# Performance work log

Hardware: AMD Instinct MI355X
Metric: run time of the kernel (lower is better)

The kernel has to match this reference:

```python
import jax, jax.numpy as jnp
import numpy as np

B, C, H, W = 4, 256, 64, 64
INTER = C // 2
BN_EPS = 1e-5


def setup_inputs() -> dict:
    key = jax.random.key(0)
    ks = jax.random.split(key, 12)
    s = 0.05
    return {
        "x": jax.random.normal(ks[0], (B, C, H, W), dtype=jnp.float32),
        "theta_w": jax.random.normal(ks[1], (INTER, C), dtype=jnp.float32) * s,
        "theta_b": jax.random.normal(ks[2], (INTER,), dtype=jnp.float32) * s,
        "phi_w": jax.random.normal(ks[3], (INTER, C), dtype=jnp.float32) * s,
        "phi_b": jax.random.normal(ks[4], (INTER,), dtype=jnp.float32) * s,
        "g_w": jax.random.normal(ks[5], (INTER, C), dtype=jnp.float32) * s,
        "g_b": jax.random.normal(ks[6], (INTER,), dtype=jnp.float32) * s,
        "W_w": jax.random.normal(ks[7], (C, INTER), dtype=jnp.float32) * s,
        "W_b": jax.random.normal(ks[8], (C,), dtype=jnp.float32) * s,
        "bn_gamma": jnp.ones((C,), dtype=jnp.float32),
        "bn_beta": jnp.zeros((C,), dtype=jnp.float32),
    }


def _conv1x1(x, w, b):
    # 1x1 conv == per-pixel GEMM: (B,C,H,W) x (O,C) -> (B,O,H,W)
    return jnp.einsum("bchw,oc->bohw", x, w) + b[None, :, None, None]


def reference(x, theta_w, theta_b, phi_w, phi_b, g_w, g_b, W_w, W_b, bn_gamma, bn_beta):
    b, c, h, w = x.shape
    hw = h * w
    theta = _conv1x1(x, theta_w, theta_b).reshape(b, -1, hw)  # (B, inter, HW) -> queries
    phi = _conv1x1(x, phi_w, phi_b).reshape(b, -1, hw)        # (B, inter, HW) -> keys
    g = _conv1x1(x, g_w, g_b).reshape(b, -1, hw)              # (B, inter, HW) -> values
    # f[n,m] = <theta[:,n], phi[:,m]> over all HW spatial positions
    f = jnp.einsum("bin,bim->bnm", theta, phi)                # (B, HW, HW)
    attn = jax.nn.softmax(f, axis=-1)
    y = jnp.einsum("bnm,bim->bin", attn, g)                   # (B, inter, HW)
    y = y.reshape(b, c // 2, h, w)
    wy = _conv1x1(y, W_w, W_b)                                # (B, C, H, W)
    # BatchNorm2d (training-mode batch statistics, per channel)
    mean = jnp.mean(wy, axis=(0, 2, 3), keepdims=True)
    var = jnp.var(wy, axis=(0, 2, 3), keepdims=True)
    wy_bn = bn_gamma[None, :, None, None] * (wy - mean) * jax.lax.rsqrt(var + BN_EPS) + bn_beta[None, :, None, None]
    return wy_bn + x
```

## Files before the change

kernel.cpp:

```cpp
#include <hip/hip_runtime.h>
#include <hip/hip_bf16.h>

#define HWN   4096
#define CIN   256
#define NINTER 128
#define NBATCH 4
#define BN_EPS 1e-5f
#define LOG2E 1.4426950408889634f
#define SMAX  64.0f

typedef __bf16 bf16_t;
typedef __bf16 bf16x8 __attribute__((ext_vector_type(8)));
typedef __bf16 bf16x4 __attribute__((ext_vector_type(4)));
typedef float  f32x4  __attribute__((ext_vector_type(4)));
typedef float  f32x16 __attribute__((ext_vector_type(16)));

__device__ __forceinline__ float fexp2(float x) {
  return __builtin_amdgcn_exp2f(x);
}

__device__ __forceinline__ void split_bf16(float v, bf16_t& h, bf16_t& l) {
  h = (bf16_t)v;
  l = (bf16_t)(v - (float)h);
}

__global__ __launch_bounds__(256) void convert_weights(
    const float* __restrict__ tw, const float* __restrict__ pw,
    const float* __restrict__ gw, const float* __restrict__ ww,
    bf16_t* __restrict__ out) {
  int i = blockIdx.x * 256 + threadIdx.x;
  float v;
  if (i < 32768)        v = tw[i];
  else if (i < 65536)   v = pw[i - 32768];
  else if (i < 98304)   v = gw[i - 65536];
  else                  v = ww[i - 98304];
  bf16_t h, l;
  split_bf16(v, h, l);
  out[i] = h;
  out[131072 + i] = l;
}

__global__ __launch_bounds__(256, 4) void qkv_kernel(
    const float* __restrict__ x, const bf16_t* __restrict__ wbf,
    const float* __restrict__ tb, const float* __restrict__ pb,
    const float* __restrict__ gb,
    bf16_t* __restrict__ Qh, bf16_t* __restrict__ Kh, bf16_t* __restrict__ V) {
  const int ntb  = blockIdx.x;
  const int b    = blockIdx.y;
  const int tid  = threadIdx.x;
  const int lane = tid & 63;
  const int wv   = tid >> 6;
  const int l31  = lane & 31;
  const int half = lane >> 5;

  __shared__ __align__(16) bf16_t smem[4608];
  bf16_t (*xTh)[72] = (bf16_t(*)[72])smem;
  bf16_t (*xTl)[72] = (bf16_t(*)[72])(smem + 2304);
  bf16_t (*Tr)[136] = (bf16_t(*)[136])smem;

  const bf16_t* Th = wbf;
  const bf16_t* Tl = wbf + 131072;
  const bf16_t* Ph = wbf + 32768;
  const bf16_t* Pl = wbf + 131072 + 32768;
  const bf16_t* Gh = wbf + 65536;
  const float*  xb = x + (size_t)b * CIN * HWN + ntb * 32;

  f32x16 aq, ak, av;
#pragma unroll
  for (int i = 0; i < 16; i++) { aq[i] = 0.f; ak[i] = 0.f; av[i] = 0.f; }

  for (int c0 = 0; c0 < 256; c0 += 64) {
    __syncthreads();
#pragma unroll
    for (int i = 0; i < 8; i++) {
      int idx = tid + i * 256;
      int cc = idx >> 5;
      int nn = idx & 31;
      float v = xb[(size_t)(c0 + cc) * HWN + nn];
      bf16_t h, l;
      split_bf16(v, h, l);
      xTh[nn][cc] = h;
      xTl[nn][cc] = l;
    }
    __syncthreads();
#pragma unroll
    for (int kk = 0; kk < 64; kk += 16) {
      size_t woff = (size_t)(32 * wv + l31) * 256 + c0 + kk + half * 8;
      bf16x8 th = *(const bf16x8*)(Th + woff);
      bf16x8 tl = *(const bf16x8*)(Tl + woff);
      bf16x8 ph = *(const bf16x8*)(Ph + woff);
      bf16x8 pl = *(const bf16x8*)(Pl + woff);
      bf16x8 gh = *(const bf16x8*)(Gh + woff);
      bf16x8 bh = *(const bf16x8*)(&xTh[l31][kk + half * 8]);
      bf16x8 bl = *(const bf16x8*)(&xTl[l31][kk + half * 8]);
      aq = __builtin_amdgcn_mfma_f32_32x32x16_bf16(th, bh, aq, 0, 0, 0);
      aq = __builtin_amdgcn_mfma_f32_32x32x16_bf16(th, bl, aq, 0, 0, 0);
      aq = __builtin_amdgcn_mfma_f32_32x32x16_bf16(tl, bh, aq, 0, 0, 0);
      ak = __builtin_amdgcn_mfma_f32_32x32x16_bf16(ph, bh, ak, 0, 0, 0);
      ak = __builtin_amdgcn_mfma_f32_32x32x16_bf16(ph, bl, ak, 0, 0, 0);
      ak = __builtin_amdgcn_mfma_f32_32x32x16_bf16(pl, bh, ak, 0, 0, 0);
      av = __builtin_amdgcn_mfma_f32_32x32x16_bf16(gh, bh, av, 0, 0, 0);
    }
  }

  const int trow = tid >> 3;
  const int tc16 = (tid & 7) * 16;
  bf16_t* qh = Qh + ((size_t)b * HWN + ntb * 32) * NINTER;
  bf16_t* kh = Kh + ((size_t)b * HWN + ntb * 32) * NINTER;

#pragma unroll
  for (int rnd = 0; rnd < 2; rnd++) {
    __syncthreads();
#pragma unroll
    for (int rg = 0; rg < 4; rg++) {
      int och0 = 32 * wv + 8 * rg + 4 * half;
#pragma unroll
      for (int j = 0; j < 4; j++) {
        float v = (rnd == 0) ? (aq[rg * 4 + j] + tb[och0 + j]) * LOG2E
                             : (ak[rg * 4 + j] + pb[och0 + j]);
        Tr[l31][och0 + j] = (bf16_t)v;
      }
    }
    __syncthreads();
    bf16_t* dst = (rnd == 0) ? qh : kh;
    bf16x8 v0 = *(const bf16x8*)(&Tr[trow][tc16]);
    bf16x8 v1 = *(const bf16x8*)(&Tr[trow][tc16 + 8]);
    *(bf16x8*)(dst + (size_t)trow * NINTER + tc16) = v0;
    *(bf16x8*)(dst + (size_t)trow * NINTER + tc16 + 8) = v1;
  }

  const int n = ntb * 32 + l31;
  bf16_t* vd = V + (size_t)b * NINTER * HWN;
#pragma unroll
  for (int r = 0; r < 16; r++) {
    int och = 32 * wv + (r & 3) + 8 * (r >> 2) + 4 * half;
    vd[(size_t)och * HWN + n] = (bf16_t)(av[r] + gb[och]);
  }
}

template<int NCv>
__global__ __launch_bounds__(256, 4) void attn_kernel(
    const bf16_t* __restrict__ Qh, const bf16_t* __restrict__ Kh,
    const bf16_t* __restrict__ V,
    float* __restrict__ Opart, float* __restrict__ Lp) {
  constexpr int CH = HWN / NCv;
  constexpr int NT = CH / 32;
  const int qt    = blockIdx.x;
  const int chunk = blockIdx.y;
  const int b     = blockIdx.z;
  const int tid   = threadIdx.x;
  const int lane  = tid & 63;
  const int wv    = tid >> 6;
  const int l15   = lane & 15;
  const int quad  = lane >> 4;
  const int kbase = chunk * CH;

  __shared__ __align__(16) bf16_t Klds[32][136];
  __shared__ __align__(16) bf16_t Vlds[144][56];
  __shared__ __align__(16) bf16_t Plds[4][32][40];

  const bf16_t* Qhb = Qh + (size_t)b * HWN * NINTER;
  const bf16_t* Khb = Kh + (size_t)b * HWN * NINTER;
  const bf16_t* Vb  = V + (size_t)b * NINTER * HWN;

  if (tid < 112) {
    int row = 128 + tid / 7;
    int c8 = (tid % 7) * 8;
    bf16x8 v;
#pragma unroll
    for (int j = 0; j < 8; j++) v[j] = (bf16_t)((row == 128) ? 1.0f : 0.0f);
    *(bf16x8*)(&Vlds[row][c8]) = v;
  }

  bf16x8 qf[2][4];
#pragma unroll
  for (int qs = 0; qs < 2; qs++) {
    const int qrow = qt * 128 + wv * 32 + qs * 16 + l15;
#pragma unroll
    for (int kc = 0; kc < 4; kc++)
      qf[qs][kc] = *(const bf16x8*)(Qhb + (size_t)qrow * NINTER + kc * 32 + quad * 8);
  }

  f32x4 o[2][8], ol[2];
#pragma unroll
  for (int qs = 0; qs < 2; qs++) {
#pragma unroll
    for (int dt = 0; dt < 8; dt++)
#pragma unroll
      for (int i = 0; i < 4; i++) o[qs][dt][i] = 0.f;
#pragma unroll
    for (int i = 0; i < 4; i++) ol[qs][i] = 0.f;
  }

  for (int t = 0; t < NT; t++) {
    __syncthreads();
#pragma unroll
    for (int i = 0; i < 2; i++) {
      int idx = tid + i * 256;
      int row = idx >> 4;
      int c8 = (idx & 15) * 8;
      *(uint4*)(&Klds[row][c8]) =
          *(const uint4*)(Khb + (size_t)(kbase + t * 32 + row) * NINTER + c8);
    }
#pragma unroll
    for (int i = 0; i < 2; i++) {
      int idx = tid + i * 256;
      int row = idx >> 2;
      int c8 = (idx & 3) * 8;
      *(uint4*)(&Vlds[row][c8]) =
          *(const uint4*)(Vb + (size_t)row * HWN + kbase + t * 32 + c8);
    }
    __syncthreads();

    f32x4 s[2][2];
#pragma unroll
    for (int qs = 0; qs < 2; qs++)
#pragma unroll
      for (int ks = 0; ks < 2; ks++)
#pragma unroll
        for (int i = 0; i < 4; i++) s[qs][ks][i] = 0.f;
#pragma unroll
    for (int ks = 0; ks < 2; ks++)
#pragma unroll
      for (int kc = 0; kc < 4; kc++) {
        bf16x8 kf = *(const bf16x8*)(&Klds[ks * 16 + l15][kc * 32 + quad * 8]);
        s[0][ks] = __builtin_amdgcn_mfma_f32_16x16x32_bf16(kf, qf[0][kc], s[0][ks], 0, 0, 0);
        s[1][ks] = __builtin_amdgcn_mfma_f32_16x16x32_bf16(kf, qf[1][kc], s[1][ks], 0, 0, 0);
      }

#pragma unroll
    for (int qs = 0; qs < 2; qs++)
#pragma unroll
      for (int ks = 0; ks < 2; ks++) {
        bf16x4 p4;
#pragma unroll
        for (int r = 0; r < 4; r++)
          p4[r] = (bf16_t)fexp2(s[qs][ks][r] - SMAX);
        *(bf16x4*)(&Plds[wv][qs * 16 + l15][ks * 16 + quad * 4]) = p4;
      }

    bf16x8 pf0 = *(const bf16x8*)(&Plds[wv][l15][quad * 8]);
    bf16x8 pf1 = *(const bf16x8*)(&Plds[wv][16 + l15][quad * 8]);
#pragma unroll
    for (int dt = 0; dt < 8; dt++) {
      bf16x8 vf = *(const bf16x8*)(&Vlds[dt * 16 + l15][quad * 8]);
      o[0][dt] = __builtin_amdgcn_mfma_f32_16x16x32_bf16(pf0, vf, o[0][dt], 0, 0, 0);
      o[1][dt] = __builtin_amdgcn_mfma_f32_16x16x32_bf16(pf1, vf, o[1][dt], 0, 0, 0);
    }
    bf16x8 vfl = *(const bf16x8*)(&Vlds[128 + l15][quad * 8]);
    ol[0] = __builtin_amdgcn_mfma_f32_16x16x32_bf16(pf0, vfl, ol[0], 0, 0, 0);
    ol[1] = __builtin_amdgcn_mfma_f32_16x16x32_bf16(pf1, vfl, ol[1], 0, 0, 0);
  }

  float* Ob = Opart + ((size_t)(b * NCv + chunk) * HWN) * NINTER;
#pragma unroll
  for (int qs = 0; qs < 2; qs++)
#pragma unroll
    for (int r = 0; r < 4; r++) {
      int n = qt * 128 + wv * 32 + qs * 16 + quad * 4 + r;
#pragma unroll
      for (int dt = 0; dt < 8; dt++)
        Ob[(size_t)n * NINTER + dt * 16 + l15] = o[qs][dt][r];
      if (l15 == 0)
        Lp[(size_t)(b * NCv + chunk) * HWN + n] = ol[qs][r];
    }
}

template<int NCv>
__global__ __launch_bounds__(256, 4) void wconv_kernel(
    const bf16_t* __restrict__ Wbf, const float* __restrict__ Opart,
    const float* __restrict__ Lp, const float* __restrict__ Wb,
    bf16_t* __restrict__ WY) {
  const int ntb = blockIdx.x;
  const int b   = blockIdx.y;
  const int tid = threadIdx.x;
  const int lane = tid & 63;
  const int wv   = tid >> 6;
  const int l31  = lane & 31;
  const int half = lane >> 5;

  __shared__ __align__(16) bf16_t Ylds[32][136];
  __shared__ float Linv[32];

  if (tid < 32) {
    int n = ntb * 32 + tid;
    float ls = 0.f;
#pragma unroll
    for (int c = 0; c < NCv; c++) ls += Lp[(size_t)(b * NCv + c) * HWN + n];
    Linv[tid] = 1.f / ls;
  }

  const int nrow = tid >> 3;
  const int dgrp = tid & 7;
  float oacc[16];
#pragma unroll
  for (int j = 0; j < 16; j++) oacc[j] = 0.f;
#pragma unroll
  for (int c = 0; c < NCv; c++) {
    const float* Op = Opart +
        ((size_t)(b * NCv + c) * HWN + ntb * 32 + nrow) * NINTER + dgrp * 16;
#pragma unroll
    for (int q = 0; q < 4; q++) {
      f32x4 v = *(const f32x4*)(Op + q * 4);
#pragma unroll
      for (int j = 0; j < 4; j++) oacc[q * 4 + j] += v[j];
    }
  }
  __syncthreads();
  {
    float inv = Linv[nrow];
    bf16x8 y0, y1;
#pragma unroll
    for (int j = 0; j < 8; j++) {
      y0[j] = (bf16_t)(oacc[j] * inv);
      y1[j] = (bf16_t)(oacc[8 + j] * inv);
    }
    *(bf16x8*)(&Ylds[nrow][dgrp * 16]) = y0;
    *(bf16x8*)(&Ylds[nrow][dgrp * 16 + 8]) = y1;
  }
  __syncthreads();

  const bf16_t* Wh = Wbf + 98304;
  f32x16 acc[2];
#pragma unroll
  for (int c = 0; c < 2; c++)
#pragma unroll
    for (int i = 0; i < 16; i++) acc[c][i] = 0.f;

#pragma unroll
  for (int k0 = 0; k0 < 128; k0 += 16) {
    bf16x8 a0 = *(const bf16x8*)(Wh + (size_t)(wv * 64 + l31) * NINTER + k0 + half * 8);
    bf16x8 a1 = *(const bf16x8*)(Wh + (size_t)(wv * 64 + 32 + l31) * NINTER + k0 + half * 8);
    bf16x8 b0 = *(const bf16x8*)(&Ylds[l31][k0 + half * 8]);
    acc[0] = __builtin_amdgcn_mfma_f32_32x32x16_bf16(a0, b0, acc[0], 0, 0, 0);
    acc[1] = __builtin_amdgcn_mfma_f32_32x32x16_bf16(a1, b0, acc[1], 0, 0, 0);
  }

  bf16_t* dst = WY + (size_t)b * 256 * HWN + ntb * 32;
#pragma unroll
  for (int ct = 0; ct < 2; ct++)
#pragma unroll
    for (int r = 0; r < 16; r++) {
      int co = wv * 64 + ct * 32 + (r & 3) + 8 * (r >> 2) + 4 * half;
      dst[(size_t)co * HWN + l31] = (bf16_t)(acc[ct][r] + Wb[co]);
    }
}

__global__ __launch_bounds__(256) void stats_kernel(
    const bf16_t* __restrict__ WY, float* __restrict__ stats) {
  const int c = blockIdx.x;
  const int tid = threadIdx.x;
  float s = 0.f, s2 = 0.f;
  for (int b = 0; b < NBATCH; b++) {
    const bf16_t* p = WY + ((size_t)b * 256 + c) * HWN;
    for (int i = tid * 8; i < HWN; i += 2048) {
      bf16x8 v8 = *(const bf16x8*)(p + i);
#pragma unroll
      for (int j = 0; j < 8; j++) {
        float v = (float)v8[j];
        s += v;
        s2 += v * v;
      }
    }
  }
#pragma unroll
  for (int off = 1; off < 64; off <<= 1) {
    s += __shfl_xor(s, off);
    s2 += __shfl_xor(s2, off);
  }
  __shared__ float red[8];
  int wv = tid >> 6;
  if ((tid & 63) == 0) { red[wv] = s; red[4 + wv] = s2; }
  __syncthreads();
  if (tid == 0) {
    float S = red[0] + red[1] + red[2] + red[3];
    float S2 = red[4] + red[5] + red[6] + red[7];
    float mean = S * (1.f / 16384.f);
    float var = S2 * (1.f / 16384.f) - mean * mean;
    stats[c] = mean;
    stats[256 + c] = rsqrtf(var + BN_EPS);
  }
}

__global__ __launch_bounds__(256) void bn_kernel(
    const bf16_t* __restrict__ WY, const float* __restrict__ x,
    const float* __restrict__ stats, const float* __restrict__ gamma,
    const float* __restrict__ beta, float* __restrict__ out) {
  int idx = blockIdx.x * 256 + threadIdx.x;
  int e = idx * 4;
  int c = (e >> 12) & 255;
  bf16x4 w4 = *(const bf16x4*)(WY + e);
  float4 xv = *(const float4*)(x + e);
  float mean = stats[c];
  float g = gamma[c] * stats[256 + c];
  float bb = beta[c];
  float4 o;
  o.x = g * ((float)w4[0] - mean) + bb + xv.x;
  o.y = g * ((float)w4[1] - mean) + bb + xv.y;
  o.z = g * ((float)w4[2] - mean) + bb + xv.z;
  o.w = g * ((float)w4[3] - mean) + bb + xv.w;
  *(float4*)(out + e) = o;
}

extern "C" void kernel_launch(void* const* d_in, const int* in_sizes, int n_in,
                              void* d_out, int out_size, void* d_ws, size_t ws_size,
                              hipStream_t stream) {
  const float* x       = (const float*)d_in[0];
  const float* theta_b = (const float*)d_in[2];
  const float* phi_b   = (const float*)d_in[4];
  const float* g_b     = (const float*)d_in[6];
  const float* W_b     = (const float*)d_in[8];
  const float* bn_g    = (const float*)d_in[9];
  const float* bn_b    = (const float*)d_in[10];
  float* out = (float*)d_out;

  const size_t NEED8 = 12582912ull + 67108864ull + 8388608ull + 524288ull +
                       524288ull + 2048ull;
  const int nc = (ws_size >= NEED8) ? 8 : 4;
  const size_t opb = (size_t)nc * HWN * NINTER * NBATCH * 4;
  const size_t lpb = (size_t)nc * HWN * NBATCH * 4;

  char* ws = (char*)d_ws;
  bf16_t* Qh  = (bf16_t*)(ws);
  bf16_t* Kh  = (bf16_t*)(ws + 4194304);
  bf16_t* V   = (bf16_t*)(ws + 8388608);
  float*  OP  = (float*)(ws + 12582912);
  bf16_t* WY  = (bf16_t*)(ws + 12582912 + opb);
  float*  LP  = (float*)(ws + 12582912 + opb + 8388608);
  bf16_t* WBF = (bf16_t*)(ws + 12582912 + opb + 8388608 + lpb);
  float*  ST  = (float*)(ws + 12582912 + opb + 8388608 + lpb + 524288);

  convert_weights<<<512, 256, 0, stream>>>(
      (const float*)d_in[1], (const float*)d_in[3],
      (const float*)d_in[5], (const float*)d_in[7], WBF);
  qkv_kernel<<<dim3(128, NBATCH), 256, 0, stream>>>(
      x, WBF, theta_b, phi_b, g_b, Qh, Kh, V);
  if (nc == 8) {
    attn_kernel<8><<<dim3(32, 8, NBATCH), 256, 0, stream>>>(Qh, Kh, V, OP, LP);
    wconv_kernel<8><<<dim3(128, NBATCH), 256, 0, stream>>>(WBF, OP, LP, W_b, WY);
  } else {
    attn_kernel<4><<<dim3(32, 4, NBATCH), 256, 0, stream>>>(Qh, Kh, V, OP, LP);
    wconv_kernel<4><<<dim3(128, NBATCH), 256, 0, stream>>>(WBF, OP, LP, W_b, WY);
  }
  stats_kernel<<<256, 256, 0, stream>>>(WY, ST);
  bn_kernel<<<4096, 256, 0, stream>>>(WY, x, ST, bn_g, bn_b, out);
}
```

Measured before the change: 213.0 us.

## Halve attention query tile per wave and fix key split at four chunks

Each wave in the attention kernel now handles 16 queries instead of 32, so a block covers 64 queries and the grid doubles along the query axis. The key-sequence split is fixed at 4 chunks instead of choosing 8 when the workspace allows, which halves the partial-output traffic written and later reduced by wconv. The launch-bounds occupancy hint drops from 4 to 2. The trade-off is that each K/V tile loaded into LDS now feeds half as many MFMAs, and every query block reloads the full K/V chunk.

Result: faster. 206.5 us (-3.1%).

```diff
diff --git a/kernel.cpp b/kernel.cpp
--- a/kernel.cpp
+++ b/kernel.cpp
@@ -139,7 +139,7 @@
 }
 
 template<int NCv>
-__global__ __launch_bounds__(256, 4) void attn_kernel(
+__global__ __launch_bounds__(256, 2) void attn_kernel(
     const bf16_t* __restrict__ Qh, const bf16_t* __restrict__ Kh,
     const bf16_t* __restrict__ V,
     float* __restrict__ Opart, float* __restrict__ Lp) {
@@ -157,7 +157,7 @@
 
   __shared__ __align__(16) bf16_t Klds[32][136];
   __shared__ __align__(16) bf16_t Vlds[144][56];
-  __shared__ __align__(16) bf16_t Plds[4][32][40];
+  __shared__ __align__(16) bf16_t Plds[4][16][40];
 
   const bf16_t* Qhb = Qh + (size_t)b * HWN * NINTER;
   const bf16_t* Khb = Kh + (size_t)b * HWN * NINTER;
@@ -172,25 +172,21 @@
     *(bf16x8*)(&Vlds[row][c8]) = v;
   }
 
-  bf16x8 qf[2][4];
-#pragma unroll
-  for (int qs = 0; qs < 2; qs++) {
-    const int qrow = qt * 128 + wv * 32 + qs * 16 + l15;
+  bf16x8 qf[4];
+  {
+    const int qrow = qt * 64 + wv * 16 + l15;
 #pragma unroll
     for (int kc = 0; kc < 4; kc++)
-      qf[qs][kc] = *(const bf16x8*)(Qhb + (size_t)qrow * NINTER + kc * 32 + quad * 8);
-  }
-
-  f32x4 o[2][8], ol[2];
-#pragma unroll
-  for (int qs = 0; qs < 2; qs++) {
-#pragma unroll
-    for (int dt = 0; dt < 8; dt++)
-#pragma unroll
-      for (int i = 0; i < 4; i++) o[qs][dt][i] = 0.f;
-#pragma unroll
-    for (int i = 0; i < 4; i++) ol[qs][i] = 0.f;
-  }
+      qf[kc] = *(const bf16x8*)(Qhb + (size_t)qrow * NINTER + kc * 32 + quad * 8);
+  }
+
+  f32x4 o[8], ol;
+#pragma unroll
+  for (int dt = 0; dt < 8; dt++)
+#pragma unroll
+    for (int i = 0; i < 4; i++) o[dt][i] = 0.f;
+#pragma unroll
+  for (int i = 0; i < 4; i++) ol[i] = 0.f;
 
   for (int t = 0; t < NT; t++) {
     __syncthreads();
@@ -212,58 +208,43 @@
     }
     __syncthreads();
 
-    f32x4 s[2][2];
-#pragma unroll
-    for (int qs = 0; qs < 2; qs++)
-#pragma unroll
-      for (int ks = 0; ks < 2; ks++)
-#pragma unroll
-        for (int i = 0; i < 4; i++) s[qs][ks][i] = 0.f;
-#pragma unroll
-    for (int ks = 0; ks < 2; ks++)
+#pragma unroll
+    for (int ks = 0; ks < 2; ks++) {
+      f32x4 s4;
+#pragma unroll
+      for (int i = 0; i < 4; i++) s4[i] = 0.f;
 #pragma unroll
       for (int kc = 0; kc < 4; kc++) {
         bf16x8 kf = *(const bf16x8*)(&Klds[ks * 16 + l15][kc * 32 + quad * 8]);
-        s[0][ks] = __builtin_amdgcn_mfma_f32_16x16x32_bf16(kf, qf[0][kc], s[0][ks], 0, 0, 0);
-        s[1][ks] = __builtin_amdgcn_mfma_f32_16x16x32_bf16(kf, qf[1][kc], s[1][ks], 0, 0, 0);
+        s4 = __builtin_amdgcn_mfma_f32_16x16x32_bf16(kf, qf[kc], s4, 0, 0, 0);
       }
-
-#pragma unroll
-    for (int qs = 0; qs < 2; qs++)
-#pragma unroll
-      for (int ks = 0; ks < 2; ks++) {
-        bf16x4 p4;
-#pragma unroll
-        for (int r = 0; r < 4; r++)
-          p4[r] = (bf16_t)fexp2(s[qs][ks][r] - SMAX);
-        *(bf16x4*)(&Plds[wv][qs * 16 + l15][ks * 16 + quad * 4]) = p4;
-      }
-
-    bf16x8 pf0 = *(const bf16x8*)(&Plds[wv][l15][quad * 8]);
-    bf16x8 pf1 = *(const bf16x8*)(&Plds[wv][16 + l15][quad * 8]);
+      bf16x4 p4;
+#pragma unroll
+      for (int r = 0; r < 4; r++)
+        p4[r] = (bf16_t)fexp2(s4[r] - SMAX);
+      *(bf16x4*)(&Plds[wv][l15][ks * 16 + quad * 4]) = p4;
+    }
+
+    bf16x8 pf = *(const bf16x8*)(&Plds[wv][l15][quad * 8]);
 #pragma unroll
     for (int dt = 0; dt < 8; dt++) {
       bf16x8 vf = *(const bf16x8*)(&Vlds[dt * 16 + l15][quad * 8]);
-      o[0][dt] = __builtin_amdgcn_mfma_f32_16x16x32_bf16(pf0, vf, o[0][dt], 0, 0, 0);
-      o[1][dt] = __builtin_amdgcn_mfma_f32_16x16x32_bf16(pf1, vf, o[1][dt], 0, 0, 0);
+      o[dt] = __builtin_amdgcn_mfma_f32_16x16x32_bf16(pf, vf, o[dt], 0, 0, 0);
     }
     bf16x8 vfl = *(const bf16x8*)(&Vlds[128 + l15][quad * 8]);
-    ol[0] = __builtin_amdgcn_mfma_f32_16x16x32_bf16(pf0, vfl, ol[0], 0, 0, 0);
-    ol[1] = __builtin_amdgcn_mfma_f32_16x16x32_bf16(pf1, vfl, ol[1], 0, 0, 0);
+    ol = __builtin_amdgcn_mfma_f32_16x16x32_bf16(pf, vfl, ol, 0, 0, 0);
   }
 
   float* Ob = Opart + ((size_t)(b * NCv + chunk) * HWN) * NINTER;
 #pragma unroll
-  for (int qs = 0; qs < 2; qs++)
-#pragma unroll
-    for (int r = 0; r < 4; r++) {
-      int n = qt * 128 + wv * 32 + qs * 16 + quad * 4 + r;
-#pragma unroll
-      for (int dt = 0; dt < 8; dt++)
-        Ob[(size_t)n * NINTER + dt * 16 + l15] = o[qs][dt][r];
-      if (l15 == 0)
-        Lp[(size_t)(b * NCv + chunk) * HWN + n] = ol[qs][r];
-    }
+  for (int r = 0; r < 4; r++) {
+    int n = qt * 64 + wv * 16 + quad * 4 + r;
+#pragma unroll
+    for (int dt = 0; dt < 8; dt++)
+      Ob[(size_t)n * NINTER + dt * 16 + l15] = o[dt][r];
+    if (l15 == 0)
+      Lp[(size_t)(b * NCv + chunk) * HWN + n] = ol[r];
+  }
 }
 
 template<int NCv>
@@ -414,11 +395,9 @@
   const float* bn_b    = (const float*)d_in[10];
   float* out = (float*)d_out;
 
-  const size_t NEED8 = 12582912ull + 67108864ull + 8388608ull + 524288ull +
-                       524288ull + 2048ull;
-  const int nc = (ws_size >= NEED8) ? 8 : 4;
-  const size_t opb = (size_t)nc * HWN * NINTER * NBATCH * 4;
-  const size_t lpb = (size_t)nc * HWN * NBATCH * 4;
+  constexpr int NC = 4;
+  const size_t opb = (size_t)NC * HWN * NINTER * NBATCH * 4;
+  const size_t lpb = (size_t)NC * HWN * NBATCH * 4;
 
   char* ws = (char*)d_ws;
   bf16_t* Qh  = (bf16_t*)(ws);
@@ -435,13 +414,10 @@
       (const float*)d_in[5], (const float*)d_in[7], WBF);
   qkv_kernel<<<dim3(128, NBATCH), 256, 0, stream>>>(
       x, WBF, theta_b, phi_b, g_b, Qh, Kh, V);
-  if (nc == 8) {
-    attn_kernel<8><<<dim3(32, 8, NBATCH), 256, 0, stream>>>(Qh, Kh, V, OP, LP);
-    wconv_kernel<8><<<dim3(128, NBATCH), 256, 0, stream>>>(WBF, OP, LP, W_b, WY);
-  } else {
-    attn_kernel<4><<<dim3(32, 4, NBATCH), 256, 0, stream>>>(Qh, Kh, V, OP, LP);
-    wconv_kernel<4><<<dim3(128, NBATCH), 256, 0, stream>>>(WBF, OP, LP, W_b, WY);
-  }
+  attn_kernel<NC><<<dim3(64, NC, NBATCH), 256, 0, stream>>>(
+      Qh, Kh, V, OP, LP);
+  wconv_kernel<NC><<<dim3(128, NBATCH), 256, 0, stream>>>(
+      WBF, OP, LP, W_b, WY);
   stats_kernel<<<256, 256, 0, stream>>>(WY, ST);
   bn_kernel<<<4096, 256, 0, stream>>>(WY, x, ST, bn_g, bn_b, out);
 }
```

## Load V fragments directly from global, prefetch K into registers, fix chunk count

Applied to the files above, without the earlier changes.

The attention kernel no longer stages V in LDS. Each lane loads its eight V fragments straight from global memory, and the row-sum column is replaced by a constant register vector of ones. K tiles are prefetched one iteration ahead in registers, so the second barrier and the global load latency move off the critical path. Launch bounds drop to 2 waves per EU to leave room for the extra registers, and the split count is fixed at 4 chunks rather than 8, giving fewer blocks and a smaller partial-output buffer at the cost of less parallelism.

Result: no change. 213.0 us (-0.0%).

```diff
diff --git a/kernel.cpp b/kernel.cpp
--- a/kernel.cpp
+++ b/kernel.cpp
@@ -139,7 +139,7 @@
 }
 
 template<int NCv>
-__global__ __launch_bounds__(256, 4) void attn_kernel(
+__global__ __launch_bounds__(256, 2) void attn_kernel(
     const bf16_t* __restrict__ Qh, const bf16_t* __restrict__ Kh,
     const bf16_t* __restrict__ V,
     float* __restrict__ Opart, float* __restrict__ Lp) {
@@ -156,21 +156,15 @@
   const int kbase = chunk * CH;
 
   __shared__ __align__(16) bf16_t Klds[32][136];
-  __shared__ __align__(16) bf16_t Vlds[144][56];
   __shared__ __align__(16) bf16_t Plds[4][32][40];
 
   const bf16_t* Qhb = Qh + (size_t)b * HWN * NINTER;
   const bf16_t* Khb = Kh + (size_t)b * HWN * NINTER;
   const bf16_t* Vb  = V + (size_t)b * NINTER * HWN;
 
-  if (tid < 112) {
-    int row = 128 + tid / 7;
-    int c8 = (tid % 7) * 8;
-    bf16x8 v;
-#pragma unroll
-    for (int j = 0; j < 8; j++) v[j] = (bf16_t)((row == 128) ? 1.0f : 0.0f);
-    *(bf16x8*)(&Vlds[row][c8]) = v;
-  }
+  bf16x8 vone;
+#pragma unroll
+  for (int j = 0; j < 8; j++) vone[j] = (bf16_t)((l15 == 0) ? 1.0f : 0.0f);
 
   bf16x8 qf[2][4];
 #pragma unroll
@@ -192,25 +186,36 @@
     for (int i = 0; i < 4; i++) ol[qs][i] = 0.f;
   }
 
+  const bf16_t* kgp = Khb + (size_t)(kbase + (tid >> 4)) * NINTER + (tid & 15) * 8;
+  const int kc8 = (tid & 15) * 8;
+  const int kr0 = tid >> 4;
+
+  const bf16_t* vgp = Vb + (size_t)l15 * HWN + kbase + quad * 8;
+
+  uint4 ka = *(const uint4*)(kgp);
+  uint4 kb = *(const uint4*)(kgp + (size_t)16 * NINTER);
+
   for (int t = 0; t < NT; t++) {
     __syncthreads();
-#pragma unroll
-    for (int i = 0; i < 2; i++) {
-      int idx = tid + i * 256;
-      int row = idx >> 4;
-      int c8 = (idx & 15) * 8;
-      *(uint4*)(&Klds[row][c8]) =
-          *(const uint4*)(Khb + (size_t)(kbase + t * 32 + row) * NINTER + c8);
-    }
-#pragma unroll
-    for (int i = 0; i < 2; i++) {
-      int idx = tid + i * 256;
-      int row = idx >> 2;
-      int c8 = (idx & 3) * 8;
-      *(uint4*)(&Vlds[row][c8]) =
-          *(const uint4*)(Vb + (size_t)row * HWN + kbase + t * 32 + c8);
-    }
-    __syncthreads();
+    *(uint4*)(&Klds[kr0][kc8]) = ka;
+    *(uint4*)(&Klds[kr0 + 16][kc8]) = kb;
+    __syncthreads();
+
+    if (t + 1 < NT) {
+      const bf16_t* kn = kgp + (size_t)(t + 1) * 32 * NINTER;
+      ka = *(const uint4*)(kn);
+      kb = *(const uint4*)(kn + (size_t)16 * NINTER);
+    }
+
+    const bf16_t* vp = vgp + t * 32;
+    bf16x8 vf0 = *(const bf16x8*)(vp);
+    bf16x8 vf1 = *(const bf16x8*)(vp + (size_t)16 * HWN);
+    bf16x8 vf2 = *(const bf16x8*)(vp + (size_t)32 * HWN);
+    bf16x8 vf3 = *(const bf16x8*)(vp + (size_t)48 * HWN);
+    bf16x8 vf4 = *(const bf16x8*)(vp + (size_t)64 * HWN);
+    bf16x8 vf5 = *(const bf16x8*)(vp + (size_t)80 * HWN);
+    bf16x8 vf6 = *(const bf16x8*)(vp + (size_t)96 * HWN);
+    bf16x8 vf7 = *(const bf16x8*)(vp + (size_t)112 * HWN);
 
     f32x4 s[2][2];
 #pragma unroll
@@ -241,15 +246,14 @@
 
     bf16x8 pf0 = *(const bf16x8*)(&Plds[wv][l15][quad * 8]);
     bf16x8 pf1 = *(const bf16x8*)(&Plds[wv][16 + l15][quad * 8]);
-#pragma unroll
-    for (int dt = 0; dt < 8; dt++) {
-      bf16x8 vf = *(const bf16x8*)(&Vlds[dt * 16 + l15][quad * 8]);
-      o[0][dt] = __builtin_amdgcn_mfma_f32_16x16x32_bf16(pf0, vf, o[0][dt], 0, 0, 0);
-      o[1][dt] = __builtin_amdgcn_mfma_f32_16x16x32_bf16(pf1, vf, o[1][dt], 0, 0, 0);
-    }
-    bf16x8 vfl = *(const bf16x8*)(&Vlds[128 + l15][quad * 8]);
-    ol[0] = __builtin_amdgcn_mfma_f32_16x16x32_bf16(pf0, vfl, ol[0], 0, 0, 0);
-    ol[1] = __builtin_amdgcn_mfma_f32_16x16x32_bf16(pf1, vfl, ol[1], 0, 0, 0);
+#define PVSTEP(i, vfi)                                                        \
+    o[0][i] = __builtin_amdgcn_mfma_f32_16x16x32_bf16(pf0, vfi, o[0][i], 0, 0, 0); \
+    o[1][i] = __builtin_amdgcn_mfma_f32_16x16x32_bf16(pf1, vfi, o[1][i], 0, 0, 0);
+    PVSTEP(0, vf0) PVSTEP(1, vf1) PVSTEP(2, vf2) PVSTEP(3, vf3)
+    PVSTEP(4, vf4) PVSTEP(5, vf5) PVSTEP(6, vf6) PVSTEP(7, vf7)
+#undef PVSTEP
+    ol[0] = __builtin_amdgcn_mfma_f32_16x16x32_bf16(pf0, vone, ol[0], 0, 0, 0);
+    ol[1] = __builtin_amdgcn_mfma_f32_16x16x32_bf16(pf1, vone, ol[1], 0, 0, 0);
   }
 
   float* Ob = Opart + ((size_t)(b * NCv + chunk) * HWN) * NINTER;
@@ -414,11 +418,9 @@
   const float* bn_b    = (const float*)d_in[10];
   float* out = (float*)d_out;
 
-  const size_t NEED8 = 12582912ull + 67108864ull + 8388608ull + 524288ull +
-                       524288ull + 2048ull;
-  const int nc = (ws_size >= NEED8) ? 8 : 4;
-  const size_t opb = (size_t)nc * HWN * NINTER * NBATCH * 4;
-  const size_t lpb = (size_t)nc * HWN * NBATCH * 4;
+  constexpr int NC = 4;
+  const size_t opb = (size_t)NC * HWN * NINTER * NBATCH * 4;
+  const size_t lpb = (size_t)NC * HWN * NBATCH * 4;
 
   char* ws = (char*)d_ws;
   bf16_t* Qh  = (bf16_t*)(ws);
@@ -435,13 +437,10 @@
       (const float*)d_in[5], (const float*)d_in[7], WBF);
   qkv_kernel<<<dim3(128, NBATCH), 256, 0, stream>>>(
       x, WBF, theta_b, phi_b, g_b, Qh, Kh, V);
-  if (nc == 8) {
-    attn_kernel<8><<<dim3(32, 8, NBATCH), 256, 0, stream>>>(Qh, Kh, V, OP, LP);
-    wconv_kernel<8><<<dim3(128, NBATCH), 256, 0, stream>>>(WBF, OP, LP, W_b, WY);
-  } else {
-    attn_kernel<4><<<dim3(32, 4, NBATCH), 256, 0, stream>>>(Qh, Kh, V, OP, LP);
-    wconv_kernel<4><<<dim3(128, NBATCH), 256, 0, stream>>>(WBF, OP, LP, W_b, WY);
-  }
+  attn_kernel<NC><<<dim3(32, NC, NBATCH), 256, 0, stream>>>(
+      Qh, Kh, V, OP, LP);
+  wconv_kernel<NC><<<dim3(128, NBATCH), 256, 0, stream>>>(
+      WBF, OP, LP, W_b, WY);
   stats_kernel<<<256, 256, 0, stream>>>(WY, ST);
   bn_kernel<<<4096, 256, 0, stream>>>(WY, x, ST, bn_g, bn_b, out);
 }
```

## Widen attention blocks to 256 queries with 8 waves and fix key split at 4

Applied to the files above, without the earlier changes.

The attention kernel now runs 512 threads (8 waves) per block covering 256 query rows, so each K/V tile staged in LDS is shared by twice as many queries and each thread does a single load per tile. The key-dimension split is fixed at 4 chunks instead of 8 when workspace allows, which halves the partial-output traffic that wconv must reduce. The grid shrinks to 16x4x4 = 256 blocks, and launch bounds change to (512,1), which loosens the register limit but may reduce occupancy and leave CUs underfilled.

Result: faster. 182.2 us (-14.5%).

```diff
diff --git a/kernel.cpp b/kernel.cpp
--- a/kernel.cpp
+++ b/kernel.cpp
@@ -139,7 +139,7 @@
 }
 
 template<int NCv>
-__global__ __launch_bounds__(256, 4) void attn_kernel(
+__global__ __launch_bounds__(512, 1) void attn_kernel(
     const bf16_t* __restrict__ Qh, const bf16_t* __restrict__ Kh,
     const bf16_t* __restrict__ V,
     float* __restrict__ Opart, float* __restrict__ Lp) {
@@ -157,7 +157,7 @@
 
   __shared__ __align__(16) bf16_t Klds[32][136];
   __shared__ __align__(16) bf16_t Vlds[144][56];
-  __shared__ __align__(16) bf16_t Plds[4][32][40];
+  __shared__ __align__(16) bf16_t Plds[8][32][40];
 
   const bf16_t* Qhb = Qh + (size_t)b * HWN * NINTER;
   const bf16_t* Khb = Kh + (size_t)b * HWN * NINTER;
@@ -175,7 +175,7 @@
   bf16x8 qf[2][4];
 #pragma unroll
   for (int qs = 0; qs < 2; qs++) {
-    const int qrow = qt * 128 + wv * 32 + qs * 16 + l15;
+    const int qrow = qt * 256 + wv * 32 + qs * 16 + l15;
 #pragma unroll
     for (int kc = 0; kc < 4; kc++)
       qf[qs][kc] = *(const bf16x8*)(Qhb + (size_t)qrow * NINTER + kc * 32 + quad * 8);
@@ -194,19 +194,15 @@
 
   for (int t = 0; t < NT; t++) {
     __syncthreads();
-#pragma unroll
-    for (int i = 0; i < 2; i++) {
-      int idx = tid + i * 256;
-      int row = idx >> 4;
-      int c8 = (idx & 15) * 8;
+    {
+      int row = tid >> 4;
+      int c8 = (tid & 15) * 8;
       *(uint4*)(&Klds[row][c8]) =
           *(const uint4*)(Khb + (size_t)(kbase + t * 32 + row) * NINTER + c8);
     }
-#pragma unroll
-    for (int i = 0; i < 2; i++) {
-      int idx = tid + i * 256;
-      int row = idx >> 2;
-      int c8 = (idx & 3) * 8;
+    {
+      int row = tid >> 2;
+      int c8 = (tid & 3) * 8;
       *(uint4*)(&Vlds[row][c8]) =
           *(const uint4*)(Vb + (size_t)row * HWN + kbase + t * 32 + c8);
     }
@@ -257,7 +253,7 @@
   for (int qs = 0; qs < 2; qs++)
 #pragma unroll
     for (int r = 0; r < 4; r++) {
-      int n = qt * 128 + wv * 32 + qs * 16 + quad * 4 + r;
+      int n = qt * 256 + wv * 32 + qs * 16 + quad * 4 + r;
 #pragma unroll
       for (int dt = 0; dt < 8; dt++)
         Ob[(size_t)n * NINTER + dt * 16 + l15] = o[qs][dt][r];
@@ -414,11 +410,9 @@
   const float* bn_b    = (const float*)d_in[10];
   float* out = (float*)d_out;
 
-  const size_t NEED8 = 12582912ull + 67108864ull + 8388608ull + 524288ull +
-                       524288ull + 2048ull;
-  const int nc = (ws_size >= NEED8) ? 8 : 4;
-  const size_t opb = (size_t)nc * HWN * NINTER * NBATCH * 4;
-  const size_t lpb = (size_t)nc * HWN * NBATCH * 4;
+  constexpr int NC = 4;
+  const size_t opb = (size_t)NC * HWN * NINTER * NBATCH * 4;
+  const size_t lpb = (size_t)NC * HWN * NBATCH * 4;
 
   char* ws = (char*)d_ws;
   bf16_t* Qh  = (bf16_t*)(ws);
@@ -435,13 +429,10 @@
       (const float*)d_in[5], (const float*)d_in[7], WBF);
   qkv_kernel<<<dim3(128, NBATCH), 256, 0, stream>>>(
       x, WBF, theta_b, phi_b, g_b, Qh, Kh, V);
-  if (nc == 8) {
-    attn_kernel<8><<<dim3(32, 8, NBATCH), 256, 0, stream>>>(Qh, Kh, V, OP, LP);
-    wconv_kernel<8><<<dim3(128, NBATCH), 256, 0, stream>>>(WBF, OP, LP, W_b, WY);
-  } else {
-    attn_kernel<4><<<dim3(32, 4, NBATCH), 256, 0, stream>>>(Qh, Kh, V, OP, LP);
-    wconv_kernel<4><<<dim3(128, NBATCH), 256, 0, stream>>>(WBF, OP, LP, W_b, WY);
-  }
+  attn_kernel<NC><<<dim3(16, NC, NBATCH), 512, 0, stream>>>(
+      Qh, Kh, V, OP, LP);
+  wconv_kernel<NC><<<dim3(128, NBATCH), 256, 0, stream>>>(
+      WBF, OP, LP, W_b, WY);
   stats_kernel<<<256, 256, 0, stream>>>(WY, ST);
   bn_kernel<<<4096, 256, 0, stream>>>(WY, x, ST, bn_g, bn_b, out);
 }
```
